# Kernel optimization log

Measured on AMD Instinct MI355X. Metric: run time of the kernel, lower is better.

The kernel has to match this reference:

```python
import jax, jax.numpy as jnp
import numpy as np

INT4_QMAX = 7.0  # symmetric int4: representable range clipped to [-8, 7]


def simulate_quantize_int4(w):
    # axis_to_reduce=None -> single global scale over the whole kernel
    scale = jnp.max(jnp.abs(w)) / INT4_QMAX
    q = jnp.clip(jnp.round(w / scale), -8.0, 7.0)
    return q * scale


def setup_inputs() -> dict:
    key = jax.random.key(0)
    k_x, k_w, k_bias, k_a, k_b = jax.random.split(key, 5)
    d_in, features, rank = 1024, 1024, 16
    x = jax.random.normal(k_x, (4, 8192, d_in), dtype=jnp.float32)
    kernel = jax.random.normal(k_w, (d_in, features), dtype=jnp.float32)
    bias = jax.random.normal(k_bias, (features,), dtype=jnp.float32)
    a = jax.random.normal(k_a, (d_in, rank), dtype=jnp.float32) * (1.0 / np.sqrt(d_in))
    b = jax.random.normal(k_b, (rank, features), dtype=jnp.float32) * 0.01
    return {"x": x, "kernel": kernel, "bias": bias, "a": a, "b": b}


def reference(x, kernel, bias, a, b):
    # fake-quantized main matmul: y = x @ dequant(quant(W)) + bias
    w = simulate_quantize_int4(kernel)
    y = jnp.einsum('bsd,df->bsf', x, w) + bias
    # LoRA adapter: x @ a @ b (contract small rank dim first)
    lora = jnp.einsum('bsr,rf->bsf', jnp.einsum('bsd,dr->bsr', x, a), b)
    return y + lora
```

## Files before the change

### kernel.cpp

```cpp
#include <hip/hip_runtime.h>
#include <hip/hip_bf16.h>

typedef __bf16 bf16x8 __attribute__((ext_vector_type(8)));
typedef __bf16 bf16x4 __attribute__((ext_vector_type(4)));
typedef float  f32x4  __attribute__((ext_vector_type(4)));

#define K_DIM 1024
#define N_DIM 1024
#define BM 128
#define BN 128
#define BK 64
#define BM2 256
#define BN2 256
#define BK2 32
#define PDEPTH 4
#define NT2 (K_DIM / BK2)

typedef unsigned int u32;
typedef u32 __attribute__((address_space(1))) u32_g;
typedef u32 __attribute__((address_space(3))) u32_s;

__device__ __forceinline__ void load16_lds(const void* g, void* s) {
    __builtin_amdgcn_global_load_lds((u32_g*)g, (u32_s*)s, 16, 0, 0);
}

__global__ void maxabs_kernel(const float* __restrict__ w, float* __restrict__ blockmax, int n4) {
    __shared__ float sm[4];
    int i = blockIdx.x * blockDim.x + threadIdx.x;
    int stride = gridDim.x * blockDim.x;
    float m = 0.f;
    for (; i < n4; i += stride) {
        float4 v = ((const float4*)w)[i];
        m = fmaxf(m, fmaxf(fmaxf(fabsf(v.x), fabsf(v.y)), fmaxf(fabsf(v.z), fabsf(v.w))));
    }
#pragma unroll
    for (int off = 32; off > 0; off >>= 1)
        m = fmaxf(m, __shfl_down(m, off, 64));
    int lane = threadIdx.x & 63, wave = threadIdx.x >> 6;
    if (lane == 0) sm[wave] = m;
    __syncthreads();
    if (threadIdx.x == 0)
        blockmax[blockIdx.x] = fmaxf(fmaxf(sm[0], sm[1]), fmaxf(sm[2], sm[3]));
}

__global__ void build_w_kernel(const float* __restrict__ kern, const float* __restrict__ amat,
                               const float* __restrict__ bmat, const float* __restrict__ blockmax,
                               __bf16* __restrict__ wt) {
    __shared__ float smax;
    if (threadIdx.x < 64) {
        float m = 0.f;
#pragma unroll
        for (int j = 0; j < 4; ++j) m = fmaxf(m, blockmax[threadIdx.x + j * 64]);
#pragma unroll
        for (int off = 32; off > 0; off >>= 1)
            m = fmaxf(m, __shfl_down(m, off, 64));
        if (threadIdx.x == 0) smax = m;
    }
    __syncthreads();
    float scale = smax * (1.0f / 7.0f);

    int t = blockIdx.x * blockDim.x + threadIdx.x;
    int k = t & (K_DIM - 1);
    int n = t >> 10;
    float w = kern[k * N_DIM + n];
    float q = rintf(w / scale);
    q = fminf(fmaxf(q, -8.f), 7.f);
    float acc = q * scale;
#pragma unroll
    for (int r = 0; r < 16; ++r)
        acc += amat[k * 16 + r] * bmat[r * N_DIM + n];
    wt[(size_t)n * K_DIM + k] = (__bf16)acc;
}

__global__ void cvt_x_kernel(const float4* __restrict__ x, bf16x8* __restrict__ xb, int n8) {
    int i = blockIdx.x * blockDim.x + threadIdx.x;
    if (i >= n8) return;
    float4 v0 = x[i * 2];
    float4 v1 = x[i * 2 + 1];
    bf16x8 o;
    o[0] = (__bf16)v0.x; o[1] = (__bf16)v0.y; o[2] = (__bf16)v0.z; o[3] = (__bf16)v0.w;
    o[4] = (__bf16)v1.x; o[5] = (__bf16)v1.y; o[6] = (__bf16)v1.z; o[7] = (__bf16)v1.w;
    xb[i] = o;
}

__global__ __launch_bounds__(512, 2)
void gemm256_kernel(const __bf16* __restrict__ xb, const __bf16* __restrict__ wt,
                    const float* __restrict__ bias, float* __restrict__ out) {
    __shared__ __attribute__((aligned(16))) __bf16 As[PDEPTH][BM2 * BK2];
    __shared__ __attribute__((aligned(16))) __bf16 Bs[PDEPTH][BN2 * BK2];

    const int tid  = threadIdx.x;
    const int lane = tid & 63;
    const int wave = tid >> 6;
    const int wr   = wave >> 2;
    const int wc   = wave & 3;
    const int l15  = lane & 15;
    const int l4   = lane >> 4;

    const int lb  = blockIdx.x;
    const int ib  = lb >> 3;
    const int bn0 = (ib & 3) * BN2;
    const int bm0 = (((ib >> 2) << 3) | (lb & 7)) * BM2;

    const int srow = lane >> 2;
    const int lc   = (lane & 3) ^ ((srow >> 1) & 3);

    const __bf16* xg = xb + (size_t)(bm0 + wave * 32 + srow) * K_DIM + lc * 8;
    const __bf16* wg = wt + (size_t)(bn0 + wave * 32 + srow) * K_DIM + lc * 8;
    __bf16* sa = &As[0][wave * 32 * BK2];
    __bf16* sb = &Bs[0][wave * 32 * BK2];

    const int ro = l15 * BK2 + ((l4 ^ ((l15 >> 1) & 3)) << 3);

    f32x4 acc[8][4] = {};

#define STAGE2(T) do {                                                     \
        const int b_ = (T) & (PDEPTH - 1); const int k_ = (T) * BK2;       \
        load16_lds(xg + k_,              sa + b_ * (BM2 * BK2));           \
        load16_lds(xg + 16 * K_DIM + k_, sa + b_ * (BM2 * BK2) + 16 * BK2);\
        load16_lds(wg + k_,              sb + b_ * (BN2 * BK2));           \
        load16_lds(wg + 16 * K_DIM + k_, sb + b_ * (BN2 * BK2) + 16 * BK2);\
    } while (0)

    STAGE2(0); STAGE2(1); STAGE2(2);

#pragma unroll 4
    for (int t = 0; t < NT2; ++t) {
        if (t < NT2 - 2)       asm volatile("s_waitcnt vmcnt(8)" ::: "memory");
        else if (t == NT2 - 2) asm volatile("s_waitcnt vmcnt(4)" ::: "memory");
        else                   asm volatile("s_waitcnt vmcnt(0)" ::: "memory");
        __builtin_amdgcn_s_barrier();
        __builtin_amdgcn_sched_barrier(0);

        if (t + 3 < NT2) STAGE2(t + 3);

        const __bf16* ap = (const __bf16*)As + (t & (PDEPTH - 1)) * (BM2 * BK2)
                           + wr * (128 * BK2) + ro;
        const __bf16* bp = (const __bf16*)Bs + (t & (PDEPTH - 1)) * (BN2 * BK2)
                           + wc * (64 * BK2) + ro;
        bf16x8 af[8], bv[4];
#pragma unroll
        for (int nt = 0; nt < 4; ++nt) bv[nt] = *(const bf16x8*)(bp + nt * (16 * BK2));
#pragma unroll
        for (int mt = 0; mt < 8; ++mt) af[mt] = *(const bf16x8*)(ap + mt * (16 * BK2));
        __builtin_amdgcn_s_setprio(1);
#pragma unroll
        for (int mt = 0; mt < 8; ++mt)
#pragma unroll
            for (int nt = 0; nt < 4; ++nt)
                acc[mt][nt] = __builtin_amdgcn_mfma_f32_16x16x32_bf16(
                    af[mt], bv[nt], acc[mt][nt], 0, 0, 0);
        __builtin_amdgcn_s_setprio(0);
    }
#undef STAGE2

#pragma unroll
    for (int nt = 0; nt < 4; ++nt) {
        int n = bn0 + wc * 64 + nt * 16 + l15;
        float bvs = bias[n];
#pragma unroll
        for (int mt = 0; mt < 8; ++mt) {
            int m = bm0 + wr * 128 + mt * 16 + l4 * 4;
            float* op = out + (size_t)m * N_DIM + n;
#pragma unroll
            for (int r = 0; r < 4; ++r)
                op[(size_t)r * N_DIM] = acc[mt][nt][r] + bvs;
        }
    }
}

__global__ __launch_bounds__(256, 4)
void gemm_fb_kernel(const float* __restrict__ x, const __bf16* __restrict__ wt,
                    const float* __restrict__ bias, float* __restrict__ out) {
    __shared__ __attribute__((aligned(16))) __bf16 As[BM * BK];
    __shared__ __attribute__((aligned(16))) __bf16 Bs[BN * BK];

    const int tid  = threadIdx.x;
    const int lane = tid & 63;
    const int wave = tid >> 6;
    const int wm = (wave >> 1) * 64;
    const int wn = (wave & 1) * 64;

    const int l = blockIdx.x;
    const int i = l >> 3;
    const int bn0 = (i & 7) * BN;
    const int bm0 = (((i >> 3) << 3) | (l & 7)) * BM;

    const int l15 = lane & 15;
    const int l4  = lane >> 4;

    f32x4 acc[4][4] = {};

    const int srow = lane >> 3;
    const int gch  = (lane & 7) ^ srow;

    for (int k0 = 0; k0 < K_DIM; k0 += BK) {
        __syncthreads();
#pragma unroll
        for (int j = 0; j < 4; ++j) {
            int r = j * 32 + wave * 8;
            const __bf16* g = wt + (size_t)(bn0 + r + srow) * K_DIM + k0 + gch * 8;
            load16_lds(g, &Bs[r * BK]);
        }
#pragma unroll
        for (int j = 0; j < 8; ++j) {
            int f  = j * 256 + tid;
            int r  = f >> 4;
            int c4 = f & 15;
            float4 v = *(const float4*)(x + (size_t)(bm0 + r) * K_DIM + k0 + c4 * 4);
            int p = (c4 >> 1) ^ (r & 7);
            bf16x4 o;
            o.x = (__bf16)v.x; o.y = (__bf16)v.y; o.z = (__bf16)v.z; o.w = (__bf16)v.w;
            *(bf16x4*)(&As[r * BK + p * 8 + (c4 & 1) * 4]) = o;
        }
        __syncthreads();

#pragma unroll
        for (int ks = 0; ks < 2; ++ks) {
            bf16x8 af[4], bfr[4];
#pragma unroll
            for (int mt = 0; mt < 4; ++mt) {
                int r = wm + mt * 16 + l15;
                int p = (ks * 4 + l4) ^ (r & 7);
                af[mt] = *(const bf16x8*)(&As[r * BK + p * 8]);
            }
#pragma unroll
            for (int nt = 0; nt < 4; ++nt) {
                int r = wn + nt * 16 + l15;
                int p = (ks * 4 + l4) ^ (r & 7);
                bfr[nt] = *(const bf16x8*)(&Bs[r * BK + p * 8]);
            }
#pragma unroll
            for (int mt = 0; mt < 4; ++mt)
#pragma unroll
                for (int nt = 0; nt < 4; ++nt)
                    acc[mt][nt] = __builtin_amdgcn_mfma_f32_16x16x32_bf16(
                        af[mt], bfr[nt], acc[mt][nt], 0, 0, 0);
        }
    }

#pragma unroll
    for (int nt = 0; nt < 4; ++nt) {
        int n = bn0 + wn + nt * 16 + l15;
        float bv = bias[n];
#pragma unroll
        for (int mt = 0; mt < 4; ++mt) {
            int m = bm0 + wm + mt * 16 + l4 * 4;
            float* op = out + (size_t)m * N_DIM + n;
#pragma unroll
            for (int r = 0; r < 4; ++r)
                op[(size_t)r * N_DIM] = acc[mt][nt][r] + bv;
        }
    }
}

extern "C" void kernel_launch(void* const* d_in, const int* in_sizes, int n_in,
                              void* d_out, int out_size, void* d_ws, size_t ws_size,
                              hipStream_t stream) {
    const float* x    = (const float*)d_in[0];
    const float* kern = (const float*)d_in[1];
    const float* bias = (const float*)d_in[2];
    const float* amat = (const float*)d_in[3];
    const float* bmat = (const float*)d_in[4];
    float* out = (float*)d_out;
    const int M = in_sizes[0] / K_DIM;

    float* blockmax = (float*)d_ws;
    __bf16* wt = (__bf16*)((char*)d_ws + 4096);
    const size_t xb_off    = 4096 + (size_t)N_DIM * K_DIM * sizeof(__bf16);
    const size_t need_fast = xb_off + (size_t)M * K_DIM * sizeof(__bf16);

    maxabs_kernel<<<256, 256, 0, stream>>>(kern, blockmax, K_DIM * N_DIM / 4);
    build_w_kernel<<<K_DIM * N_DIM / 256, 256, 0, stream>>>(kern, amat, bmat, blockmax, wt);

    if (ws_size >= need_fast && (M % (BM2 * 8)) == 0) {
        __bf16* xbuf = (__bf16*)((char*)d_ws + xb_off);
        int n8 = M * K_DIM / 8;
        cvt_x_kernel<<<(n8 + 255) / 256, 256, 0, stream>>>((const float4*)x, (bf16x8*)xbuf, n8);
        gemm256_kernel<<<(M / BM2) * (N_DIM / BN2), 512, 0, stream>>>(xbuf, wt, bias, out);
    } else {
        gemm_fb_kernel<<<(M / BM) * (N_DIM / BN), 256, 0, stream>>>(x, wt, bias, out);
    }
}
```

Measured before the change: 336.9 us.

## Split main-loop iteration into four interleaved LDS-read/global-load/MFMA phases

Restructures the GEMM main loop into four sub-phases. Each phase reads a subset of A/B fragments from LDS, issues one global-to-LDS load for the stage three tiles ahead, and runs an 8-MFMA block, with barriers between phases. The aim is to spread global loads and LDS reads across the MFMA work (ping-pong style) instead of bursting them at the top of each iteration, and to lower register pressure by holding half-size fragment arrays. In exchange it adds several barriers per iteration and uses more intricate vmcnt accounting for the tail, which risks added synchronization stalls.

```diff
diff --git a/kernel.cpp b/kernel.cpp
--- a/kernel.cpp
+++ b/kernel.cpp
@@ -114,7 +114,7 @@
 
     f32x4 acc[8][4] = {};
 
-#define STAGE2(T) do {                                                     \
+#define STAGE_ALL(T) do {                                                  \
         const int b_ = (T) & (PDEPTH - 1); const int k_ = (T) * BK2;       \
         load16_lds(xg + k_,              sa + b_ * (BM2 * BK2));           \
         load16_lds(xg + 16 * K_DIM + k_, sa + b_ * (BM2 * BK2) + 16 * BK2);\
@@ -122,37 +122,83 @@
         load16_lds(wg + 16 * K_DIM + k_, sb + b_ * (BN2 * BK2) + 16 * BK2);\
     } while (0)
 
-    STAGE2(0); STAGE2(1); STAGE2(2);
+    STAGE_ALL(0); STAGE_ALL(1); STAGE_ALL(2);
+    asm volatile("s_waitcnt vmcnt(8)" ::: "memory");
+    __builtin_amdgcn_s_barrier();
 
 #pragma unroll 4
     for (int t = 0; t < NT2; ++t) {
-        if (t < NT2 - 2)       asm volatile("s_waitcnt vmcnt(8)" ::: "memory");
-        else if (t == NT2 - 2) asm volatile("s_waitcnt vmcnt(4)" ::: "memory");
-        else                   asm volatile("s_waitcnt vmcnt(0)" ::: "memory");
-        __builtin_amdgcn_s_barrier();
-        __builtin_amdgcn_sched_barrier(0);
-
-        if (t + 3 < NT2) STAGE2(t + 3);
-
-        const __bf16* ap = (const __bf16*)As + (t & (PDEPTH - 1)) * (BM2 * BK2)
-                           + wr * (128 * BK2) + ro;
-        const __bf16* bp = (const __bf16*)Bs + (t & (PDEPTH - 1)) * (BN2 * BK2)
-                           + wc * (64 * BK2) + ro;
-        bf16x8 af[8], bv[4];
-#pragma unroll
-        for (int nt = 0; nt < 4; ++nt) bv[nt] = *(const bf16x8*)(bp + nt * (16 * BK2));
-#pragma unroll
-        for (int mt = 0; mt < 8; ++mt) af[mt] = *(const bf16x8*)(ap + mt * (16 * BK2));
+        const int buf = t & (PDEPTH - 1);
+        const int stb = (t + 3) & (PDEPTH - 1);
+        const int k_  = (t + 3) * BK2;
+        const bool st = (t + 3) < NT2;
+        const __bf16* ap = (const __bf16*)As + buf * (BM2 * BK2) + wr * (128 * BK2) + ro;
+        const __bf16* bp = (const __bf16*)Bs + buf * (BN2 * BK2) + wc * (64 * BK2) + ro;
+        bf16x8 af[4], bv0[2], bv1[2];
+
+#pragma unroll
+        for (int mt = 0; mt < 4; ++mt) af[mt] = *(const bf16x8*)(ap + mt * (16 * BK2));
+#pragma unroll
+        for (int nt = 0; nt < 2; ++nt) bv0[nt] = *(const bf16x8*)(bp + nt * (16 * BK2));
+        if (st) load16_lds(xg + k_, sa + stb * (BM2 * BK2));
+        __builtin_amdgcn_s_barrier();
+        asm volatile("s_waitcnt lgkmcnt(0)");
         __builtin_amdgcn_s_setprio(1);
 #pragma unroll
-        for (int mt = 0; mt < 8; ++mt)
-#pragma unroll
-            for (int nt = 0; nt < 4; ++nt)
+        for (int mt = 0; mt < 4; ++mt)
+#pragma unroll
+            for (int nt = 0; nt < 2; ++nt)
                 acc[mt][nt] = __builtin_amdgcn_mfma_f32_16x16x32_bf16(
-                    af[mt], bv[nt], acc[mt][nt], 0, 0, 0);
+                    af[mt], bv0[nt], acc[mt][nt], 0, 0, 0);
         __builtin_amdgcn_s_setprio(0);
-    }
-#undef STAGE2
+        __builtin_amdgcn_s_barrier();
+
+#pragma unroll
+        for (int nt = 0; nt < 2; ++nt) bv1[nt] = *(const bf16x8*)(bp + (32 + nt * 16) * BK2);
+        if (st) load16_lds(xg + 16 * K_DIM + k_, sa + stb * (BM2 * BK2) + 16 * BK2);
+        __builtin_amdgcn_s_barrier();
+        asm volatile("s_waitcnt lgkmcnt(0)");
+        __builtin_amdgcn_s_setprio(1);
+#pragma unroll
+        for (int mt = 0; mt < 4; ++mt)
+#pragma unroll
+            for (int nt = 0; nt < 2; ++nt)
+                acc[mt][2 + nt] = __builtin_amdgcn_mfma_f32_16x16x32_bf16(
+                    af[mt], bv1[nt], acc[mt][2 + nt], 0, 0, 0);
+        __builtin_amdgcn_s_setprio(0);
+        __builtin_amdgcn_s_barrier();
+
+#pragma unroll
+        for (int mt = 0; mt < 4; ++mt) af[mt] = *(const bf16x8*)(ap + (64 + mt * 16) * BK2);
+        if (st) load16_lds(wg + k_, sb + stb * (BN2 * BK2));
+        __builtin_amdgcn_s_barrier();
+        asm volatile("s_waitcnt lgkmcnt(0)");
+        __builtin_amdgcn_s_setprio(1);
+#pragma unroll
+        for (int mt = 0; mt < 4; ++mt)
+#pragma unroll
+            for (int nt = 0; nt < 2; ++nt)
+                acc[4 + mt][nt] = __builtin_amdgcn_mfma_f32_16x16x32_bf16(
+                    af[mt], bv0[nt], acc[4 + mt][nt], 0, 0, 0);
+        __builtin_amdgcn_s_setprio(0);
+        __builtin_amdgcn_s_barrier();
+
+        if (st) load16_lds(wg + 16 * K_DIM + k_, sb + stb * (BN2 * BK2) + 16 * BK2);
+        __builtin_amdgcn_s_barrier();
+        __builtin_amdgcn_s_setprio(1);
+#pragma unroll
+        for (int mt = 0; mt < 4; ++mt)
+#pragma unroll
+            for (int nt = 0; nt < 2; ++nt)
+                acc[4 + mt][2 + nt] = __builtin_amdgcn_mfma_f32_16x16x32_bf16(
+                    af[mt], bv1[nt], acc[4 + mt][2 + nt], 0, 0, 0);
+        __builtin_amdgcn_s_setprio(0);
+        if (t < NT2 - 3)       asm volatile("s_waitcnt vmcnt(8)" ::: "memory");
+        else if (t == NT2 - 3) asm volatile("s_waitcnt vmcnt(4)" ::: "memory");
+        else if (t == NT2 - 2) asm volatile("s_waitcnt vmcnt(0)" ::: "memory");
+        __builtin_amdgcn_s_barrier();
+    }
+#undef STAGE_ALL
 
 #pragma unroll
     for (int nt = 0; nt < 4; ++nt) {
```

After: 337.9 us. No clear change (+0.3%).

## Interleave LDS fragment reads, global prefetch and MFMA phases in GEMM main loop

Applied to the files above, without the earlier changes.

Rewrites the bf16 GEMM main loop so each K-step is split into three MFMA phases. Fine-grained lgkmcnt waits let the first MFMAs start once only part of the LDS fragments has arrived. The A and B global-to-LDS prefetches are issued separately between phases, and the loop runs two steps per iteration with no tail branches. The prefetch index wraps with the K index, so the last steps issue redundant loads instead of branching. The goal is more overlap of LDS latency and memory issue with matrix math, at the cost of some wasted tail bandwidth and stricter reliance on exact wait counts.

```diff
diff --git a/kernel.cpp b/kernel.cpp
--- a/kernel.cpp
+++ b/kernel.cpp
@@ -13,8 +13,9 @@
 #define BM2 256
 #define BN2 256
 #define BK2 32
-#define PDEPTH 4
 #define NT2 (K_DIM / BK2)
+#define AS_T (BM2 * BK2)
+#define BS_T (BN2 * BK2)
 
 typedef unsigned int u32;
 typedef u32 __attribute__((address_space(1))) u32_g;
@@ -86,8 +87,8 @@
 __global__ __launch_bounds__(512, 2)
 void gemm256_kernel(const __bf16* __restrict__ xb, const __bf16* __restrict__ wt,
                     const float* __restrict__ bias, float* __restrict__ out) {
-    __shared__ __attribute__((aligned(16))) __bf16 As[PDEPTH][BM2 * BK2];
-    __shared__ __attribute__((aligned(16))) __bf16 Bs[PDEPTH][BN2 * BK2];
+    __shared__ __attribute__((aligned(16))) __bf16 As[4][AS_T];
+    __shared__ __attribute__((aligned(16))) __bf16 Bs[4][BS_T];
 
     const int tid  = threadIdx.x;
     const int lane = tid & 63;
@@ -114,45 +115,71 @@
 
     f32x4 acc[8][4] = {};
 
-#define STAGE2(T) do {                                                     \
-        const int b_ = (T) & (PDEPTH - 1); const int k_ = (T) * BK2;       \
-        load16_lds(xg + k_,              sa + b_ * (BM2 * BK2));           \
-        load16_lds(xg + 16 * K_DIM + k_, sa + b_ * (BM2 * BK2) + 16 * BK2);\
-        load16_lds(wg + k_,              sb + b_ * (BN2 * BK2));           \
-        load16_lds(wg + 16 * K_DIM + k_, sb + b_ * (BN2 * BK2) + 16 * BK2);\
+#define STAGE_A(T) do { int b_ = (T) & 3; int k_ = ((T) & 31) * BK2;        \
+        load16_lds(xg + k_,              sa + b_ * AS_T);                   \
+        load16_lds(xg + 16 * K_DIM + k_, sa + b_ * AS_T + 16 * BK2); } while (0)
+#define STAGE_B(T) do { int b_ = (T) & 3; int k_ = ((T) & 31) * BK2;        \
+        load16_lds(wg + k_,              sb + b_ * BS_T);                   \
+        load16_lds(wg + 16 * K_DIM + k_, sb + b_ * BS_T + 16 * BK2); } while (0)
+
+#define HALF(BUFI, ST) do {                                                  \
+        const int buf_ = (BUFI);                                             \
+        const __bf16* ap = (const __bf16*)As + buf_ * AS_T + wr * (128 * BK2) + ro; \
+        const __bf16* bp = (const __bf16*)Bs + buf_ * BS_T + wc * (64 * BK2) + ro;  \
+        bf16x8 af[8], bv[4];                                                 \
+        af[0] = *(const bf16x8*)(ap + 0 * (16 * BK2));                       \
+        af[1] = *(const bf16x8*)(ap + 1 * (16 * BK2));                       \
+        af[2] = *(const bf16x8*)(ap + 2 * (16 * BK2));                       \
+        af[3] = *(const bf16x8*)(ap + 3 * (16 * BK2));                       \
+        bv[0] = *(const bf16x8*)(bp + 0 * (16 * BK2));                       \
+        bv[1] = *(const bf16x8*)(bp + 1 * (16 * BK2));                       \
+        af[4] = *(const bf16x8*)(ap + 4 * (16 * BK2));                       \
+        af[5] = *(const bf16x8*)(ap + 5 * (16 * BK2));                       \
+        af[6] = *(const bf16x8*)(ap + 6 * (16 * BK2));                       \
+        af[7] = *(const bf16x8*)(ap + 7 * (16 * BK2));                       \
+        bv[2] = *(const bf16x8*)(bp + 2 * (16 * BK2));                       \
+        bv[3] = *(const bf16x8*)(bp + 3 * (16 * BK2));                       \
+        STAGE_A(ST);                                                         \
+        asm volatile("s_waitcnt lgkmcnt(6)" ::: "memory");                   \
+        __builtin_amdgcn_sched_barrier(0);                                   \
+        __builtin_amdgcn_s_setprio(1);                                       \
+        _Pragma("unroll") for (int mt = 0; mt < 4; ++mt)                     \
+        _Pragma("unroll") for (int nt = 0; nt < 2; ++nt)                     \
+            acc[mt][nt] = __builtin_amdgcn_mfma_f32_16x16x32_bf16(           \
+                af[mt], bv[nt], acc[mt][nt], 0, 0, 0);                       \
+        asm volatile("s_waitcnt lgkmcnt(2)" ::: "memory");                   \
+        __builtin_amdgcn_sched_barrier(0);                                   \
+        _Pragma("unroll") for (int mt = 4; mt < 8; ++mt)                     \
+        _Pragma("unroll") for (int nt = 0; nt < 2; ++nt)                     \
+            acc[mt][nt] = __builtin_amdgcn_mfma_f32_16x16x32_bf16(           \
+                af[mt], bv[nt], acc[mt][nt], 0, 0, 0);                       \
+        STAGE_B(ST);                                                         \
+        asm volatile("s_waitcnt lgkmcnt(0)" ::: "memory");                   \
+        __builtin_amdgcn_sched_barrier(0);                                   \
+        _Pragma("unroll") for (int mt = 0; mt < 8; ++mt)                     \
+        _Pragma("unroll") for (int nt = 2; nt < 4; ++nt)                     \
+            acc[mt][nt] = __builtin_amdgcn_mfma_f32_16x16x32_bf16(           \
+                af[mt], bv[nt], acc[mt][nt], 0, 0, 0);                       \
+        __builtin_amdgcn_s_setprio(0);                                       \
+        asm volatile("s_waitcnt vmcnt(8)" ::: "memory");                     \
+        __builtin_amdgcn_s_barrier();                                        \
     } while (0)
 
-    STAGE2(0); STAGE2(1); STAGE2(2);
-
-#pragma unroll 4
-    for (int t = 0; t < NT2; ++t) {
-        if (t < NT2 - 2)       asm volatile("s_waitcnt vmcnt(8)" ::: "memory");
-        else if (t == NT2 - 2) asm volatile("s_waitcnt vmcnt(4)" ::: "memory");
-        else                   asm volatile("s_waitcnt vmcnt(0)" ::: "memory");
-        __builtin_amdgcn_s_barrier();
-        __builtin_amdgcn_sched_barrier(0);
-
-        if (t + 3 < NT2) STAGE2(t + 3);
-
-        const __bf16* ap = (const __bf16*)As + (t & (PDEPTH - 1)) * (BM2 * BK2)
-                           + wr * (128 * BK2) + ro;
-        const __bf16* bp = (const __bf16*)Bs + (t & (PDEPTH - 1)) * (BN2 * BK2)
-                           + wc * (64 * BK2) + ro;
-        bf16x8 af[8], bv[4];
-#pragma unroll
-        for (int nt = 0; nt < 4; ++nt) bv[nt] = *(const bf16x8*)(bp + nt * (16 * BK2));
-#pragma unroll
-        for (int mt = 0; mt < 8; ++mt) af[mt] = *(const bf16x8*)(ap + mt * (16 * BK2));
-        __builtin_amdgcn_s_setprio(1);
-#pragma unroll
-        for (int mt = 0; mt < 8; ++mt)
-#pragma unroll
-            for (int nt = 0; nt < 4; ++nt)
-                acc[mt][nt] = __builtin_amdgcn_mfma_f32_16x16x32_bf16(
-                    af[mt], bv[nt], acc[mt][nt], 0, 0, 0);
-        __builtin_amdgcn_s_setprio(0);
-    }
-#undef STAGE2
+    STAGE_A(0); STAGE_B(0);
+    STAGE_A(1); STAGE_B(1);
+    STAGE_A(2); STAGE_B(2);
+    asm volatile("s_waitcnt vmcnt(8)" ::: "memory");
+    __builtin_amdgcn_s_barrier();
+
+#pragma unroll 1
+    for (int u = 0; u < NT2 / 2; ++u) {
+        const int t0 = 2 * u;
+        HALF(t0 & 3, t0 + 3);
+        HALF((t0 + 1) & 3, t0 + 4);
+    }
+#undef HALF
+#undef STAGE_A
+#undef STAGE_B
 
 #pragma unroll
     for (int nt = 0; nt < 4; ++nt) {
```

Measured after the change: 317.2 us. -5.8%, faster.
